# Performance work log

Measured on AMD Instinct MI355X. Metric: run time of the kernel, lower is better.

## Reference

```python
import jax, jax.numpy as jnp
import numpy as np

# FP4 E2M1 lookup table: low 3 bits = magnitude code, bit 3 = sign
E2M1_LUT = jnp.array([0.0, 0.5, 1.0, 1.5, 2.0, 3.0, 4.0, 6.0,
                      -0.0, -0.5, -1.0, -1.5, -2.0, -3.0, -4.0, -6.0],
                     dtype=jnp.float32)

INNER_BLOCK = 16    # elements per fp8 (e4m3) inner scale
OUTER_BLOCK = 128   # elements per fp32 outlier scale


def dequant_fp4(w_q, w_os, w_is):
    """Dequantize packed FP4 weights.
    w_q : [out, in//2] int (uint8 semantics: two nibbles per byte)
    w_os: [out, in//128] fp32 outlier scales
    w_is: [out, in//16]  fp32 values on the fp8 e4m3 grid (inner scales)
    returns W: [out, in] fp32
    """
    out_f = w_q.shape[0]
    lo = E2M1_LUT[w_q & 0xF]          # even in-feature indices
    hi = E2M1_LUT[(w_q >> 4) & 0xF]   # odd in-feature indices
    w = jnp.stack([lo, hi], axis=-1).reshape(out_f, -1)  # [out, in]
    w = w * jnp.repeat(w_is, INNER_BLOCK, axis=1)
    w = w * jnp.repeat(w_os, OUTER_BLOCK, axis=1)
    return w


def setup_inputs() -> dict:
    key = jax.random.key(0)
    k1, k2, k3, k4 = jax.random.split(key, 4)
    M, IN, OUT = 8192, 4096, 16384

    x = jax.random.normal(k1, (M, IN), dtype=jnp.float32)

    # packed FP4 codes (uint8 semantics, stored as int32 for portability)
    w_q = jax.random.randint(k2, (OUT, IN // 2), 0, 256, dtype=jnp.int32)

    # per-128-block fp32 outlier scales (positive)
    w_os = jax.random.uniform(k3, (OUT, IN // OUTER_BLOCK), dtype=jnp.float32,
                              minval=0.001, maxval=0.01)

    # per-16-block inner scales, snapped to the fp8 e4m3 grid
    w_is_raw = jax.random.uniform(k4, (OUT, IN // INNER_BLOCK), dtype=jnp.float32,
                                  minval=0.25, maxval=2.0)
    w_is = w_is_raw.astype(jnp.float8_e4m3fn).astype(jnp.float32)

    # transposed dequantized weight, exactly consistent (used by backward)
    w_t = dequant_fp4(w_q, w_os, w_is).T  # [IN, OUT]

    return {"x": x, "w_q": w_q, "w_os": w_os, "w_is": w_is, "w_t": w_t}


def reference(x, w_q, w_os, w_is, w_t):
    # x.float() + flatten-to-2D already satisfied by setup (x is [M, in] fp32).
    w = dequant_fp4(w_q, w_os, w_is)          # [out, in]
    y = jnp.einsum('mk,nk->mn', x, w)         # fused dequant + GEMM math
    return y
```

## Files before the change

### kernel.cpp

```cpp
#include <hip/hip_runtime.h>
#include <hip/hip_bf16.h>
#include <stdint.h>
#include <stddef.h>

#define M_DIM 8192
#define K_DIM 4096
#define N_DIM 16384

#define BM 256
#define BN 256
#define BK 64
#define KT (K_DIM / BK)
#define SLOT_SH (BM * BK)

typedef __attribute__((ext_vector_type(8))) short bf16x8;
typedef __attribute__((ext_vector_type(4))) float f32x4;
typedef __attribute__((ext_vector_type(4))) int   i32x4;

static __device__ __forceinline__ short f2bf(float f) {
    union { float f; uint32_t u; } v; v.f = f;
    uint32_t r = v.u + 0x7FFFu + ((v.u >> 16) & 1u);
    return (short)(r >> 16);
}

static __device__ __forceinline__ float e2m1(int v) {
    int e = (v >> 1) & 3;
    int m = v & 1;
    float mag = (e == 0) ? 0.5f * (float)m
                         : (float)(2 + m) * 0.25f * (float)(1 << e);
    return (v & 8) ? -mag : mag;
}

static __device__ __forceinline__ void gload16(short* lds, const short* g) {
    __builtin_amdgcn_global_load_lds(
        (const __attribute__((address_space(1))) void*)g,
        (__attribute__((address_space(3))) void*)lds,
        16, 0, 0);
}

__global__ void cast_x_kernel(const float* __restrict__ x, short* __restrict__ xb) {
    size_t i = (size_t)blockIdx.x * 256 + threadIdx.x;
    const float4* s = reinterpret_cast<const float4*>(x);
    float4 a = s[2 * i];
    float4 b = s[2 * i + 1];
    bf16x8 o;
    o[0] = f2bf(a.x); o[1] = f2bf(a.y); o[2] = f2bf(a.z); o[3] = f2bf(a.w);
    o[4] = f2bf(b.x); o[5] = f2bf(b.y); o[6] = f2bf(b.z); o[7] = f2bf(b.w);
    reinterpret_cast<bf16x8*>(xb)[i] = o;
}

__global__ void dequant_w_kernel(const int* __restrict__ wq,
                                 const float* __restrict__ wos,
                                 const float* __restrict__ wis,
                                 short* __restrict__ wb) {
    int tid = blockIdx.x * 256 + threadIdx.x;
    int n   = tid >> 8;
    int blk = tid & 255;
    float scale = wis[(n << 8) | blk] * wos[(n << 5) | (blk >> 3)];
    const i32x4* q = reinterpret_cast<const i32x4*>(wq + ((size_t)n << 11) + (blk << 3));
    i32x4 q0 = q[0], q1 = q[1];
    bf16x8 o0, o1;
#pragma unroll
    for (int j = 0; j < 4; ++j) {
        int c = q0[j];
        o0[2 * j]     = f2bf(e2m1(c & 15) * scale);
        o0[2 * j + 1] = f2bf(e2m1((c >> 4) & 15) * scale);
    }
#pragma unroll
    for (int j = 0; j < 4; ++j) {
        int c = q1[j];
        o1[2 * j]     = f2bf(e2m1(c & 15) * scale);
        o1[2 * j + 1] = f2bf(e2m1((c >> 4) & 15) * scale);
    }
    bf16x8* dst = reinterpret_cast<bf16x8*>(wb) + 2 * (size_t)tid;
    dst[0] = o0;
    dst[1] = o1;
}

__global__ __launch_bounds__(512)
void gemm_bt_kernel(const short* __restrict__ A,
                    const short* __restrict__ B,
                    float* __restrict__ C) {
    __shared__ __align__(16) short As[2 * SLOT_SH];
    __shared__ __align__(16) short Bs[2 * SLOT_SH];

    int bid = blockIdx.x;
    int xcd = bid & 7;
    int idx = bid >> 3;
    int im  = idx >> 3;
    int in8 = idx & 7;
    int bm  = im << 8;
    int bn  = ((xcd << 3) + in8) << 8;

    int t    = threadIdx.x;
    int lane = t & 63;
    int w    = t >> 6;
    int wm   = w >> 2;
    int wn   = w & 3;
    int fr   = lane & 15;
    int fq   = lane >> 4;
    int wbase = w << 9;

    int gcol = (((t & 7) ^ ((t >> 3) & 7)) << 3);
    const short* AgB = A + (size_t)(bm + (t >> 3)) * K_DIM + gcol;
    const short* BgB = B + (size_t)(bn + (t >> 3)) * K_DIM + gcol;

    int s0 = fq ^ (fr & 7);
    int s1 = s0 ^ 4;
    int aBase = ((wm << 7) + fr) * 8;
    int bBase = ((wn << 6) + fr) * 8;

    f32x4 acc[8][4] = {};

#define STAGE_A(slot_, kt_)                                                   \
    do {                                                                      \
        const short* _s = AgB + (size_t)(kt_) * BK;                           \
        short* _d = As + (slot_) * SLOT_SH + wbase;                           \
        gload16(_d,         _s);                                              \
        gload16(_d + 4096,  _s + (size_t)64  * K_DIM);                        \
        gload16(_d + 8192,  _s + (size_t)128 * K_DIM);                        \
        gload16(_d + 12288, _s + (size_t)192 * K_DIM);                        \
    } while (0)
#define STAGE_B(slot_, kt_)                                                   \
    do {                                                                      \
        const short* _s = BgB + (size_t)(kt_) * BK;                           \
        short* _d = Bs + (slot_) * SLOT_SH + wbase;                           \
        gload16(_d,         _s);                                              \
        gload16(_d + 4096,  _s + (size_t)64  * K_DIM);                        \
        gload16(_d + 8192,  _s + (size_t)128 * K_DIM);                        \
        gload16(_d + 12288, _s + (size_t)192 * K_DIM);                        \
    } while (0)

    STAGE_A(0, 0);
    STAGE_B(0, 0);
    asm volatile("s_waitcnt vmcnt(0)" ::: "memory");
    __builtin_amdgcn_s_barrier();

    for (int kt = 0; kt < KT; ++kt) {
        int c     = kt & 1;
        int nslot = c ^ 1;
        int ktn   = (kt + 1) & (KT - 1);
        const bf16x8* Af = reinterpret_cast<const bf16x8*>(As + c * SLOT_SH);
        const bf16x8* Bf = reinterpret_cast<const bf16x8*>(Bs + c * SLOT_SH);

        STAGE_A(nslot, ktn);
        STAGE_B(nslot, ktn);

        bf16x8 av[4], aw[4], bv[4];

#pragma unroll
        for (int ni = 0; ni < 4; ++ni) bv[ni] = Bf[bBase + ni * 128 + s0];
#pragma unroll
        for (int mi = 0; mi < 4; ++mi) av[mi] = Af[aBase + mi * 128 + s0];
        __builtin_amdgcn_s_setprio(1);
#pragma unroll
        for (int mi = 0; mi < 4; ++mi)
#pragma unroll
            for (int ni = 0; ni < 4; ++ni)
                acc[mi][ni] = __builtin_amdgcn_mfma_f32_16x16x32_bf16(
                    av[mi], bv[ni], acc[mi][ni], 0, 0, 0);
        __builtin_amdgcn_s_setprio(0);

#pragma unroll
        for (int mi = 0; mi < 4; ++mi) aw[mi] = Af[aBase + (mi + 4) * 128 + s0];
        __builtin_amdgcn_s_setprio(1);
#pragma unroll
        for (int mi = 0; mi < 4; ++mi)
#pragma unroll
            for (int ni = 0; ni < 4; ++ni)
                acc[mi + 4][ni] = __builtin_amdgcn_mfma_f32_16x16x32_bf16(
                    aw[mi], bv[ni], acc[mi + 4][ni], 0, 0, 0);
        __builtin_amdgcn_s_setprio(0);

#pragma unroll
        for (int ni = 0; ni < 4; ++ni) bv[ni] = Bf[bBase + ni * 128 + s1];
#pragma unroll
        for (int mi = 0; mi < 4; ++mi) av[mi] = Af[aBase + mi * 128 + s1];
        __builtin_amdgcn_s_setprio(1);
#pragma unroll
        for (int mi = 0; mi < 4; ++mi)
#pragma unroll
            for (int ni = 0; ni < 4; ++ni)
                acc[mi][ni] = __builtin_amdgcn_mfma_f32_16x16x32_bf16(
                    av[mi], bv[ni], acc[mi][ni], 0, 0, 0);
        __builtin_amdgcn_s_setprio(0);

#pragma unroll
        for (int mi = 0; mi < 4; ++mi) aw[mi] = Af[aBase + (mi + 4) * 128 + s1];
        __builtin_amdgcn_s_setprio(1);
#pragma unroll
        for (int mi = 0; mi < 4; ++mi)
#pragma unroll
            for (int ni = 0; ni < 4; ++ni)
                acc[mi + 4][ni] = __builtin_amdgcn_mfma_f32_16x16x32_bf16(
                    aw[mi], bv[ni], acc[mi + 4][ni], 0, 0, 0);
        __builtin_amdgcn_s_setprio(0);

        asm volatile("s_waitcnt vmcnt(0)" ::: "memory");
        __builtin_amdgcn_s_barrier();
    }
#undef STAGE_A
#undef STAGE_B

#pragma unroll
    for (int mi = 0; mi < 8; ++mi) {
#pragma unroll
        for (int j = 0; j < 4; ++j) {
            size_t row = (size_t)(bm + (wm << 7) + mi * 16 + fq * 4 + j);
            float* Crow = C + row * N_DIM + (bn + (wn << 6) + fr);
#pragma unroll
            for (int ni = 0; ni < 4; ++ni)
                Crow[ni * 16] = acc[mi][ni][j];
        }
    }
}

extern "C" void kernel_launch(void* const* d_in, const int* in_sizes, int n_in,
                              void* d_out, int out_size, void* d_ws, size_t ws_size,
                              hipStream_t stream) {
    const float* x   = (const float*)d_in[0];
    const int*   wq  = (const int*)d_in[1];
    const float* wos = (const float*)d_in[2];
    const float* wis = (const float*)d_in[3];
    float* out = (float*)d_out;

    short* xb = (short*)d_ws;
    short* wb = (short*)((char*)d_ws + (size_t)M_DIM * K_DIM * 2);

    cast_x_kernel<<<(M_DIM * (size_t)K_DIM / 8) / 256, 256, 0, stream>>>(x, xb);
    dequant_w_kernel<<<(N_DIM * (size_t)K_DIM / 16) / 256, 256, 0, stream>>>(wq, wos, wis, wb);
    gemm_bt_kernel<<<(M_DIM / BM) * (N_DIM / BN), 512, 0, stream>>>(xb, wb, out);
}
```

Baseline: 1.237 ms.

## Software-pipeline LDS fragment loads across MFMA groups with register double-buffering

```diff
diff --git a/kernel.cpp b/kernel.cpp
--- a/kernel.cpp
+++ b/kernel.cpp
@@ -131,73 +131,88 @@
         gload16(_d + 12288, _s + (size_t)192 * K_DIM);                        \
     } while (0)
 
+    bf16x8 aB0[4], aB1[4], bB0[4], bB1[4];
+
     STAGE_A(0, 0);
     STAGE_B(0, 0);
     asm volatile("s_waitcnt vmcnt(0)" ::: "memory");
     __builtin_amdgcn_s_barrier();
+    {
+        const bf16x8* Af = reinterpret_cast<const bf16x8*>(As);
+        const bf16x8* Bf = reinterpret_cast<const bf16x8*>(Bs);
+#pragma unroll
+        for (int ni = 0; ni < 4; ++ni) bB0[ni] = Bf[bBase + ni * 128 + s0];
+#pragma unroll
+        for (int mi = 0; mi < 4; ++mi) aB0[mi] = Af[aBase + mi * 128 + s0];
+    }
 
     for (int kt = 0; kt < KT; ++kt) {
-        int c     = kt & 1;
-        int nslot = c ^ 1;
-        int ktn   = (kt + 1) & (KT - 1);
-        const bf16x8* Af = reinterpret_cast<const bf16x8*>(As + c * SLOT_SH);
-        const bf16x8* Bf = reinterpret_cast<const bf16x8*>(Bs + c * SLOT_SH);
-
-        STAGE_A(nslot, ktn);
-        STAGE_B(nslot, ktn);
-
-        bf16x8 av[4], aw[4], bv[4];
-
-#pragma unroll
-        for (int ni = 0; ni < 4; ++ni) bv[ni] = Bf[bBase + ni * 128 + s0];
-#pragma unroll
-        for (int mi = 0; mi < 4; ++mi) av[mi] = Af[aBase + mi * 128 + s0];
+        int c   = kt & 1;
+        int ktn = (kt + 1) & (KT - 1);
+        const bf16x8* Af  = reinterpret_cast<const bf16x8*>(As + c * SLOT_SH);
+        const bf16x8* Bf  = reinterpret_cast<const bf16x8*>(Bs + c * SLOT_SH);
+        const bf16x8* AfN = reinterpret_cast<const bf16x8*>(As + (c ^ 1) * SLOT_SH);
+        const bf16x8* BfN = reinterpret_cast<const bf16x8*>(Bs + (c ^ 1) * SLOT_SH);
+
+        STAGE_A(c ^ 1, ktn);
+        STAGE_B(c ^ 1, ktn);
+
+#pragma unroll
+        for (int mi = 0; mi < 4; ++mi) aB1[mi] = Af[aBase + (mi + 4) * 128 + s0];
+        __builtin_amdgcn_sched_barrier(0);
         __builtin_amdgcn_s_setprio(1);
 #pragma unroll
         for (int mi = 0; mi < 4; ++mi)
 #pragma unroll
             for (int ni = 0; ni < 4; ++ni)
                 acc[mi][ni] = __builtin_amdgcn_mfma_f32_16x16x32_bf16(
-                    av[mi], bv[ni], acc[mi][ni], 0, 0, 0);
-        __builtin_amdgcn_s_setprio(0);
-
-#pragma unroll
-        for (int mi = 0; mi < 4; ++mi) aw[mi] = Af[aBase + (mi + 4) * 128 + s0];
+                    aB0[mi], bB0[ni], acc[mi][ni], 0, 0, 0);
+        __builtin_amdgcn_s_setprio(0);
+
+#pragma unroll
+        for (int mi = 0; mi < 4; ++mi) aB0[mi] = Af[aBase + mi * 128 + s1];
+#pragma unroll
+        for (int ni = 0; ni < 4; ++ni) bB1[ni] = Bf[bBase + ni * 128 + s1];
+        __builtin_amdgcn_sched_barrier(0);
         __builtin_amdgcn_s_setprio(1);
 #pragma unroll
         for (int mi = 0; mi < 4; ++mi)
 #pragma unroll
             for (int ni = 0; ni < 4; ++ni)
                 acc[mi + 4][ni] = __builtin_amdgcn_mfma_f32_16x16x32_bf16(
-                    aw[mi], bv[ni], acc[mi + 4][ni], 0, 0, 0);
-        __builtin_amdgcn_s_setprio(0);
-
-#pragma unroll
-        for (int ni = 0; ni < 4; ++ni) bv[ni] = Bf[bBase + ni * 128 + s1];
-#pragma unroll
-        for (int mi = 0; mi < 4; ++mi) av[mi] = Af[aBase + mi * 128 + s1];
+                    aB1[mi], bB0[ni], acc[mi + 4][ni], 0, 0, 0);
+        __builtin_amdgcn_s_setprio(0);
+
+#pragma unroll
+        for (int mi = 0; mi < 4; ++mi) aB1[mi] = Af[aBase + (mi + 4) * 128 + s1];
+        __builtin_amdgcn_sched_barrier(0);
         __builtin_amdgcn_s_setprio(1);
 #pragma unroll
         for (int mi = 0; mi < 4; ++mi)
 #pragma unroll
             for (int ni = 0; ni < 4; ++ni)
                 acc[mi][ni] = __builtin_amdgcn_mfma_f32_16x16x32_bf16(
-                    av[mi], bv[ni], acc[mi][ni], 0, 0, 0);
-        __builtin_amdgcn_s_setprio(0);
-
-#pragma unroll
-        for (int mi = 0; mi < 4; ++mi) aw[mi] = Af[aBase + (mi + 4) * 128 + s1];
-        __builtin_amdgcn_s_setprio(1);
-#pragma unroll
-        for (int mi = 0; mi < 4; ++mi)
-#pragma unroll
-            for (int ni = 0; ni < 4; ++ni)
-                acc[mi + 4][ni] = __builtin_amdgcn_mfma_f32_16x16x32_bf16(
-                    aw[mi], bv[ni], acc[mi + 4][ni], 0, 0, 0);
-        __builtin_amdgcn_s_setprio(0);
-
+                    aB0[mi], bB1[ni], acc[mi][ni], 0, 0, 0);
+        __builtin_amdgcn_s_setprio(0);
+
+        asm volatile("s_waitcnt lgkmcnt(0)" ::: "memory");
+        __builtin_amdgcn_sched_barrier(0);
         asm volatile("s_waitcnt vmcnt(0)" ::: "memory");
         __builtin_amdgcn_s_barrier();
+
+#pragma unroll
+        for (int ni = 0; ni < 4; ++ni) bB0[ni] = BfN[bBase + ni * 128 + s0];
+#pragma unroll
+        for (int mi = 0; mi < 4; ++mi) aB0[mi] = AfN[aBase + mi * 128 + s0];
+        __builtin_amdgcn_sched_barrier(0);
+        __builtin_amdgcn_s_setprio(1);
+#pragma unroll
+        for (int mi = 0; mi < 4; ++mi)
+#pragma unroll
+            for (int ni = 0; ni < 4; ++ni)
+                acc[mi + 4][ni] = __builtin_amdgcn_mfma_f32_16x16x32_bf16(
+                    aB1[mi], bB1[ni], acc[mi + 4][ni], 0, 0, 0);
+        __builtin_amdgcn_s_setprio(0);
     }
 #undef STAGE_A
 #undef STAGE_B
```

After: 1.168 ms. -5.7%, faster.
